# Optimization experiments

Hardware: AMD Instinct MI355X
Metric: run time of the kernel (lower is better)

Reference implementation:

```python
import jax, jax.numpy as jnp
import numpy as np

B, T, E = 2, 2048, 1024
H = 16
DH = E // H  # 64
DFF = 4 * E
EPS = 1e-5


def _layernorm(x, gamma, beta):
    mu = jnp.mean(x, axis=-1, keepdims=True)
    var = jnp.mean((x - mu) ** 2, axis=-1, keepdims=True)
    return (x - mu) * jax.lax.rsqrt(var + EPS) * gamma + beta


def setup_inputs() -> dict:
    key = jax.random.key(0)
    ks = jax.random.split(key, 16)
    s_e = 1.0 / np.sqrt(E)
    s_f = 1.0 / np.sqrt(DFF)
    return {
        "x": jax.random.normal(ks[0], (B, T, E), jnp.float32),
        # per-head QKV projections, stacked over heads [H, E, DH]
        "Wq": jax.random.normal(ks[1], (H, E, DH), jnp.float32) * s_e,
        "bq": jnp.zeros((H, DH), jnp.float32),
        "Wk": jax.random.normal(ks[2], (H, E, DH), jnp.float32) * s_e,
        "bk": jnp.zeros((H, DH), jnp.float32),
        "Wv": jax.random.normal(ks[3], (H, E, DH), jnp.float32) * s_e,
        "bv": jnp.zeros((H, DH), jnp.float32),
        # output projection
        "Wo": jax.random.normal(ks[4], (E, E), jnp.float32) * s_e,
        "bo": jnp.zeros((E,), jnp.float32),
        # feed-forward
        "W1": jax.random.normal(ks[5], (E, DFF), jnp.float32) * s_e,
        "b1": jnp.zeros((DFF,), jnp.float32),
        "W2": jax.random.normal(ks[6], (DFF, E), jnp.float32) * s_f,
        "b2": jnp.zeros((E,), jnp.float32),
        # layernorms
        "gamma1": jnp.ones((E,), jnp.float32),
        "beta1": jnp.zeros((E,), jnp.float32),
        "gamma2": jnp.ones((E,), jnp.float32),
        "beta2": jnp.zeros((E,), jnp.float32),
    }


def reference(x, Wq, bq, Wk, bk, Wv, bv, Wo, bo, W1, b1, W2, b2,
              gamma1, beta1, gamma2, beta2):
    Bc, Tc, Ec = x.shape
    # --- multi-head causal self-attention (dropout = eval/identity) ---
    xn = _layernorm(x, gamma1, beta1)
    q = jnp.einsum('bte,hed->bhtd', xn, Wq) + bq[:, None, :]
    k = jnp.einsum('bte,hed->bhtd', xn, Wk) + bk[:, None, :]
    v = jnp.einsum('bte,hed->bhtd', xn, Wv) + bv[:, None, :]
    scale = 1.0 / np.sqrt(q.shape[-1])
    scores = jnp.einsum('bhtd,bhsd->bhts', q, k) * scale  # [B,H,T,T]
    causal = jnp.tril(jnp.ones((Tc, Tc), bool))
    scores = jnp.where(causal, scores, jnp.float32(-1e9))
    attn = jax.nn.softmax(scores, axis=-1)
    out = jnp.einsum('bhts,bhsd->bhtd', attn, v)          # [B,H,T,DH]
    out = out.transpose(0, 2, 1, 3).reshape(Bc, Tc, Ec)    # concat heads
    out = out @ Wo + bo
    x = x + out
    # --- feed-forward ---
    xn2 = _layernorm(x, gamma2, beta2)
    h = jax.nn.relu(xn2 @ W1 + b1)
    x = x + (h @ W2 + b2)
    return x
```

## Files before the change

kernel.cpp:

```cpp
#include <hip/hip_runtime.h>
#include <stdint.h>

#define BT    4096
#define EDIM  1024
#define TLEN  2048
#define NH    16
#define DHH   64
#define DFFN  4096

typedef short short8 __attribute__((ext_vector_type(8)));
typedef float f32x4  __attribute__((ext_vector_type(4)));

typedef const __attribute__((address_space(1))) unsigned int* gas_ptr;
typedef __attribute__((address_space(3))) unsigned int*       las_ptr;

__device__ __forceinline__ float bf2f(unsigned short u) {
    union { unsigned int i; float f; } c; c.i = ((unsigned int)u) << 16; return c.f;
}
__device__ __forceinline__ unsigned short f2bf(float f) {
    union { float f; unsigned int i; } c; c.f = f;
    unsigned int u = c.i;
    unsigned int r = u + 0x7fffu + ((u >> 16) & 1u);
    return (unsigned short)(r >> 16);
}
__device__ __forceinline__ unsigned short f2bf_trunc(float f) {
    union { float f; unsigned int i; } c; c.f = f;
    return (unsigned short)(c.i >> 16);
}
__device__ __forceinline__ float fexp2(float x) {
#if __has_builtin(__builtin_amdgcn_exp2f)
    return __builtin_amdgcn_exp2f(x);
#else
    return __expf(x * 0.69314718056f);
#endif
}
__device__ __forceinline__ void gload16(const unsigned short* g, unsigned short* l) {
    __builtin_amdgcn_global_load_lds((gas_ptr)g, (las_ptr)l, 16, 0, 0);
}

template<int QKV>
__global__ __launch_bounds__(256) void transpose_kernel(
    const float* src, unsigned short* dst, int Kdim, int srcStride)
{
    __shared__ float T[64][65];
    int t = threadIdx.x;
    int n0 = blockIdx.x * 64, k0 = blockIdx.y * 64;
    int r = t >> 4, c4 = (t & 15) * 4;
    #pragma unroll
    for (int i = 0; i < 4; i++) {
        int rr = r + i * 16;
        const float* p;
        if (QKV) p = src + ((size_t)(n0 >> 6)) * 65536 + (size_t)(k0 + rr) * 64 + c4;
        else     p = src + (size_t)(k0 + rr) * srcStride + n0 + c4;
        float4 v = *(const float4*)p;
        T[c4 + 0][rr] = v.x;
        T[c4 + 1][rr] = v.y;
        T[c4 + 2][rr] = v.z;
        T[c4 + 3][rr] = v.w;
    }
    __syncthreads();
    int rn = t >> 2, ck = (t & 3) * 16;
    short8 o0, o1;
    #pragma unroll
    for (int j = 0; j < 8; j++) o0[j] = (short)f2bf(T[rn][ck + j]);
    #pragma unroll
    for (int j = 0; j < 8; j++) o1[j] = (short)f2bf(T[rn][ck + 8 + j]);
    unsigned short* dp = dst + (size_t)(n0 + rn) * Kdim + k0 + ck;
    *(short8*)dp       = o0;
    *(short8*)(dp + 8) = o1;
}

__global__ __launch_bounds__(256) void transpose_qkv3_kernel(
    const float* __restrict__ Wq, const float* __restrict__ Wk,
    const float* __restrict__ Wv, unsigned short* __restrict__ dstbase)
{
    __shared__ float T[64][65];
    int z = blockIdx.z;
    const float* src = (z == 0) ? Wq : (z == 1) ? Wk : Wv;
    unsigned short* dst = dstbase + (size_t)z * 1048576;
    int t = threadIdx.x;
    int n0 = blockIdx.x * 64, k0 = blockIdx.y * 64;
    int r = t >> 4, c4 = (t & 15) * 4;
    #pragma unroll
    for (int i = 0; i < 4; i++) {
        int rr = r + i * 16;
        const float* p = src + ((size_t)(n0 >> 6)) * 65536 + (size_t)(k0 + rr) * 64 + c4;
        float4 v = *(const float4*)p;
        T[c4 + 0][rr] = v.x;
        T[c4 + 1][rr] = v.y;
        T[c4 + 2][rr] = v.z;
        T[c4 + 3][rr] = v.w;
    }
    __syncthreads();
    int rn = t >> 2, ck = (t & 3) * 16;
    short8 o0, o1;
    #pragma unroll
    for (int j = 0; j < 8; j++) o0[j] = (short)f2bf(T[rn][ck + j]);
    #pragma unroll
    for (int j = 0; j < 8; j++) o1[j] = (short)f2bf(T[rn][ck + 8 + j]);
    unsigned short* dp = dst + (size_t)(n0 + rn) * EDIM + k0 + ck;
    *(short8*)dp       = o0;
    *(short8*)(dp + 8) = o1;
}

__global__ __launch_bounds__(256) void transpose_ffn_kernel(
    const float* __restrict__ W1h, const float* __restrict__ W2h,
    unsigned short* __restrict__ w1t, unsigned short* __restrict__ w2t)
{
    __shared__ float T[64][65];
    int z = blockIdx.z;
    const float* src;
    unsigned short* dst;
    int Kdim, sstride, n0, k0;
    if (z == 0) { src = W1h; dst = w1t; Kdim = 1024; sstride = 4096;
                  n0 = blockIdx.x * 64; k0 = blockIdx.y * 64; }
    else        { src = W2h; dst = w2t; Kdim = 2048; sstride = 1024;
                  n0 = blockIdx.y * 64; k0 = blockIdx.x * 64; }
    int t = threadIdx.x;
    int r = t >> 4, c4 = (t & 15) * 4;
    #pragma unroll
    for (int i = 0; i < 4; i++) {
        int rr = r + i * 16;
        const float* p = src + (size_t)(k0 + rr) * sstride + n0 + c4;
        float4 v = *(const float4*)p;
        T[c4 + 0][rr] = v.x;
        T[c4 + 1][rr] = v.y;
        T[c4 + 2][rr] = v.z;
        T[c4 + 3][rr] = v.w;
    }
    __syncthreads();
    int rn = t >> 2, ck = (t & 3) * 16;
    short8 o0, o1;
    #pragma unroll
    for (int j = 0; j < 8; j++) o0[j] = (short)f2bf(T[rn][ck + j]);
    #pragma unroll
    for (int j = 0; j < 8; j++) o1[j] = (short)f2bf(T[rn][ck + 8 + j]);
    unsigned short* dp = dst + (size_t)(n0 + rn) * Kdim + k0 + ck;
    *(short8*)dp       = o0;
    *(short8*)(dp + 8) = o1;
}

__global__ __launch_bounds__(256) void vtrans_kernel(
    const unsigned short* __restrict__ v, unsigned short* __restrict__ vt)
{
    __shared__ __align__(16) unsigned short T[64][72];
    int bh = blockIdx.x, st = blockIdx.y;
    int t = threadIdx.x;
    int r = t >> 2, c = (t & 3) * 16;
    const unsigned short* src = v + ((size_t)bh * TLEN + st * 64) * DHH;
    short8 a0 = *(const short8*)(src + r * DHH + c);
    short8 a1 = *(const short8*)(src + r * DHH + c + 8);
    *(short8*)&T[r][c]     = a0;
    *(short8*)&T[r][c + 8] = a1;
    __syncthreads();
    int d = t >> 2;
    short8 o0, o1;
    #pragma unroll
    for (int j = 0; j < 8; j++) o0[j] = (short)T[c + j][d];
    #pragma unroll
    for (int j = 0; j < 8; j++) o1[j] = (short)T[c + 8 + j][d];
    unsigned short* dst = vt + ((size_t)bh * DHH + d) * TLEN + st * 64 + c;
    *(short8*)dst       = o0;
    *(short8*)(dst + 8) = o1;
}

__global__ __launch_bounds__(256) void bias_fuse_kernel(
    const float* __restrict__ bq, const float* __restrict__ bk,
    const float* __restrict__ bv, float* __restrict__ dst)
{
    int t = blockIdx.x * 256 + threadIdx.x;
    const float* src = (t < 1024) ? bq : (t < 2048) ? bk : bv;
    dst[t] = src[t & 1023];
}

template<int F32IN>
__global__ __launch_bounds__(256) void ln_fused_kernel(
    const void* __restrict__ x, const float* __restrict__ g,
    const float* __restrict__ b, unsigned short* __restrict__ out)
{
    int row = blockIdx.x, tid = threadIdx.x;
    size_t off = (size_t)row * EDIM + tid * 4;
    float v0, v1, v2, v3;
    if (F32IN) {
        float4 a = *(const float4*)((const float*)x + off);
        v0 = a.x; v1 = a.y; v2 = a.z; v3 = a.w;
    } else {
        ushort4 raw = *(const ushort4*)((const unsigned short*)x + off);
        v0 = bf2f(raw.x); v1 = bf2f(raw.y); v2 = bf2f(raw.z); v3 = bf2f(raw.w);
    }
    float s  = v0 + v1 + v2 + v3;
    float ss = v0*v0 + v1*v1 + v2*v2 + v3*v3;
    #pragma unroll
    for (int o = 1; o < 64; o <<= 1) {
        s  += __shfl_xor(s,  o, 64);
        ss += __shfl_xor(ss, o, 64);
    }
    __shared__ float red[8];
    int wave = tid >> 6;
    if ((tid & 63) == 0) { red[wave*2] = s; red[wave*2+1] = ss; }
    __syncthreads();
    s  = red[0] + red[2] + red[4] + red[6];
    ss = red[1] + red[3] + red[5] + red[7];
    float m  = s * (1.0f / EDIM);
    float rs = rsqrtf(ss * (1.0f / EDIM) - m * m + 1e-5f);
    float4 gv = *(const float4*)(g + tid * 4);
    float4 bv = *(const float4*)(b + tid * 4);
    ushort4 o;
    o.x = f2bf((v0 - m) * rs * gv.x + bv.x);
    o.y = f2bf((v1 - m) * rs * gv.y + bv.y);
    o.z = f2bf((v2 - m) * rs * gv.z + bv.z);
    o.w = f2bf((v3 - m) * rs * gv.w + bv.w);
    *(ushort4*)(out + off) = o;
}

#define V_QKV  0
#define V_WO   1
#define V_FF1  2
#define V_FF2A 3
#define V_FF2B 4

template<int VARIANT, int BN>
__global__ __launch_bounds__(256) void gemm_bt_kernel(
    const unsigned short* A,
    const unsigned short* Bt,
    const float* bias,
    const void* resid,
    void* out,
    int N, int K)
{
    constexpr int NJ = BN / 32;
    __shared__ __align__(16) unsigned short As[128 * 64];
    __shared__ __align__(16) unsigned short Bs[BN * 64];
    int tid  = threadIdx.x;
    int lane = tid & 63, wave = tid >> 6;
    int quad = lane >> 4, l16 = lane & 15;
    int wr = wave >> 1, wc = wave & 1;
    int m0 = blockIdx.y * 128, n0 = blockIdx.x * BN;

    f32x4 acc[4][NJ];
    #pragma unroll
    for (int i = 0; i < 4; i++)
        #pragma unroll
        for (int j = 0; j < NJ; j++) acc[i][j] = (f32x4){0.f, 0.f, 0.f, 0.f};

    int lr = lane >> 3;
    int lc = (lane & 7) * 8;

    for (int k0 = 0; k0 < K; k0 += 64) {
        #pragma unroll
        for (int i = 0; i < 4; i++) {
            int r = (i * 4 + wave) * 8 + lr;
            gload16(A + (size_t)(m0 + r) * K + k0 + lc, &As[(i * 4 + wave) * 512]);
        }
        #pragma unroll
        for (int i = 0; i < NJ; i++) {
            int r = (i * 4 + wave) * 8 + lr;
            gload16(Bt + (size_t)(n0 + r) * K + k0 + lc, &Bs[(i * 4 + wave) * 512]);
        }
        __syncthreads();

        #pragma unroll
        for (int ks = 0; ks < 2; ks++) {
            short8 af[4], bf[NJ];
            #pragma unroll
            for (int i = 0; i < 4; i++)
                af[i] = *(const short8*)(&As[(wr * 64 + i * 16 + l16) * 64 + ks * 32 + quad * 8]);
            #pragma unroll
            for (int j = 0; j < NJ; j++)
                bf[j] = *(const short8*)(&Bs[(wc * (BN / 2) + j * 16 + l16) * 64 + ks * 32 + quad * 8]);
            #pragma unroll
            for (int i = 0; i < 4; i++)
                #pragma unroll
                for (int j = 0; j < NJ; j++)
                    acc[i][j] = __builtin_amdgcn_mfma_f32_16x16x32_bf16(af[i], bf[j], acc[i][j], 0, 0, 0);
        }

        __syncthreads();
    }

    #pragma unroll
    for (int j = 0; j < NJ; j++) {
        int c = n0 + wc * (BN / 2) + j * 16 + l16;
        float bi = (VARIANT == V_FF2A) ? 0.0f : bias[c];
        #pragma unroll
        for (int i = 0; i < 4; i++) {
            #pragma unroll
            for (int r = 0; r < 4; r++) {
                int m = m0 + wr * 64 + i * 16 + quad * 4 + r;
                float val = acc[i][j][r] + bi;
                if (VARIANT == V_WO)
                    val += ((const float*)resid)[(size_t)m * N + c];
                if (VARIANT == V_FF2B)
                    val += bf2f(((const unsigned short*)resid)[(size_t)m * N + c])
                         + ((const float*)out)[(size_t)m * N + c];
                if (VARIANT == V_FF1)
                    val = fmaxf(val, 0.0f);
                if (VARIANT == V_QKV) {
                    int b = m >> 11, t = m & 2047;
                    int mat = c >> 10, cc = c & 1023;
                    int h = cc >> 6, d = cc & 63;
                    ((unsigned short*)out)[(size_t)mat * 4194304 +
                        (((size_t)(b * NH + h)) * TLEN + t) * DHH + d] = f2bf(val);
                } else if (VARIANT == V_FF2A || VARIANT == V_FF2B) {
                    ((float*)out)[(size_t)m * N + c] = val;
                } else {
                    ((unsigned short*)out)[(size_t)m * N + c] = f2bf(val);
                }
            }
        }
    }
}

__global__ __launch_bounds__(256) void attn_kernel(
    const unsigned short* __restrict__ q,
    const unsigned short* __restrict__ k,
    const unsigned short* __restrict__ vt,
    unsigned short* __restrict__ att)
{
    __shared__ __align__(16) unsigned short Ks[128 * 72];
    __shared__ __align__(16) unsigned short Vs[64 * 136];
    __shared__ __align__(16) unsigned short Ps[4][16 * 136];
    int tid  = threadIdx.x;
    int lane = tid & 63, wave = tid >> 6;
    int quad = lane >> 4, l16 = lane & 15;

    int flat = blockIdx.x;
    int xcd  = flat & 7, idx = flat >> 3;
    int bh   = xcd * 4 + (idx >> 5);
    int qt   = 31 - (idx & 31);
    int q0   = qt * 64;
    int qw   = q0 + wave * 16;

    const unsigned short* Qb = q  + ((size_t)bh * TLEN + qw) * DHH;
    const unsigned short* Kb = k  + (size_t)bh * TLEN * DHH;
    const unsigned short* Vb = vt + (size_t)bh * DHH * TLEN;

    short8 aq0 = *(const short8*)(Qb + l16 * DHH + quad * 8);
    short8 aq1 = *(const short8*)(Qb + l16 * DHH + 32 + quad * 8);

    f32x4 o[4];
    #pragma unroll
    for (int n = 0; n < 4; n++) o[n] = (f32x4){0.f, 0.f, 0.f, 0.f};
    f32x4 mrow = {-1e30f, -1e30f, -1e30f, -1e30f};
    f32x4 lrow = {0.f, 0.f, 0.f, 0.f};
    unsigned short* Pw = Ps[wave];
    const float cs = 0.18033688011f;

    int rowK = tid >> 1, colK = (tid & 1) * 32;
    int rowV = tid >> 2, colV = (tid & 3) * 32;

    int nch = (q0 >> 7) + 1;

    short8 ka0, ka1, ka2, ka3, va0, va1, va2, va3;
    {
        const unsigned short* kp = Kb + (size_t)rowK * DHH + colK;
        ka0 = *(const short8*)kp;
        ka1 = *(const short8*)(kp + 8);
        ka2 = *(const short8*)(kp + 16);
        ka3 = *(const short8*)(kp + 24);
        const unsigned short* vp = Vb + (size_t)rowV * TLEN + colV;
        va0 = *(const short8*)vp;
        va1 = *(const short8*)(vp + 8);
        va2 = *(const short8*)(vp + 16);
        va3 = *(const short8*)(vp + 24);
    }

    for (int ch = 0; ch < nch; ch++) {
        int s0 = ch * 128;
        __syncthreads();
        *(short8*)(&Ks[rowK * 72 + colK])       = ka0;
        *(short8*)(&Ks[rowK * 72 + colK + 8])   = ka1;
        *(short8*)(&Ks[rowK * 72 + colK + 16])  = ka2;
        *(short8*)(&Ks[rowK * 72 + colK + 24])  = ka3;
        *(short8*)(&Vs[rowV * 136 + colV])      = va0;
        *(short8*)(&Vs[rowV * 136 + colV + 8])  = va1;
        *(short8*)(&Vs[rowV * 136 + colV + 16]) = va2;
        *(short8*)(&Vs[rowV * 136 + colV + 24]) = va3;
        __syncthreads();

        if (ch + 1 < nch) {
            int s1 = s0 + 128;
            const unsigned short* kp = Kb + (size_t)(s1 + rowK) * DHH + colK;
            ka0 = *(const short8*)kp;
            ka1 = *(const short8*)(kp + 8);
            ka2 = *(const short8*)(kp + 16);
            ka3 = *(const short8*)(kp + 24);
            const unsigned short* vp = Vb + (size_t)rowV * TLEN + s1 + colV;
            va0 = *(const short8*)vp;
            va1 = *(const short8*)(vp + 8);
            va2 = *(const short8*)(vp + 16);
            va3 = *(const short8*)(vp + 24);
        }

        f32x4 S[8];
        #pragma unroll
        for (int n = 0; n < 8; n++) {
            short8 b0 = *(const short8*)(&Ks[(n * 16 + l16) * 72 + quad * 8]);
            short8 b1 = *(const short8*)(&Ks[(n * 16 + l16) * 72 + 32 + quad * 8]);
            f32x4 s = (f32x4){0.f, 0.f, 0.f, 0.f};
            s = __builtin_amdgcn_mfma_f32_16x16x32_bf16(aq0, b0, s, 0, 0, 0);
            s = __builtin_amdgcn_mfma_f32_16x16x32_bf16(aq1, b1, s, 0, 0, 0);
            S[n] = s;
        }
        bool needmask = (s0 + 127 > qw);
        #pragma unroll
        for (int r = 0; r < 4; r++) {
            float xv[8];
            #pragma unroll
            for (int n = 0; n < 8; n++) {
                float xx = S[n][r] * cs;
                if (needmask && (s0 + n * 16 + l16 > qw + quad * 4 + r)) xx = -1e30f;
                xv[n] = xx;
            }
            float mxl = fmaxf(fmaxf(fmaxf(xv[0], xv[1]), fmaxf(xv[2], xv[3])),
                              fmaxf(fmaxf(xv[4], xv[5]), fmaxf(xv[6], xv[7])));
            float used;
            if (__all(mxl <= mrow[r] + 8.0f)) {
                used = mrow[r];
            } else {
                float mx = mxl;
                mx = fmaxf(mx, __shfl_xor(mx, 1, 64));
                mx = fmaxf(mx, __shfl_xor(mx, 2, 64));
                mx = fmaxf(mx, __shfl_xor(mx, 4, 64));
                mx = fmaxf(mx, __shfl_xor(mx, 8, 64));
                float mnew  = fmaxf(mrow[r], mx);
                float alpha = fexp2(mrow[r] - mnew);
                lrow[r] *= alpha;
                o[0][r] *= alpha; o[1][r] *= alpha;
                o[2][r] *= alpha; o[3][r] *= alpha;
                mrow[r] = mnew;
                used = mnew;
            }
            float ps = 0.f;
            int prow = (quad * 4 + r) * 136;
            #pragma unroll
            for (int n = 0; n < 8; n++) {
                float p = fexp2(xv[n] - used);
                ps += p;
                Pw[prow + n * 16 + l16] = f2bf_trunc(p);
            }
            lrow[r] += ps;
        }
        short8 ap[4];
        #pragma unroll
        for (int ks = 0; ks < 4; ks++)
            ap[ks] = *(const short8*)(Pw + l16 * 136 + ks * 32 + quad * 8);
        #pragma unroll
        for (int n = 0; n < 4; n++) {
            #pragma unroll
            for (int ks = 0; ks < 4; ks++) {
                short8 b = *(const short8*)(&Vs[(n * 16 + l16) * 136 + ks * 32 + quad * 8]);
                o[n] = __builtin_amdgcn_mfma_f32_16x16x32_bf16(ap[ks], b, o[n], 0, 0, 0);
            }
        }
    }

    int bidx = bh >> 4, hh = bh & 15;
    #pragma unroll
    for (int r = 0; r < 4; r++) {
        float ls = lrow[r];
        ls += __shfl_xor(ls, 1, 64);
        ls += __shfl_xor(ls, 2, 64);
        ls += __shfl_xor(ls, 4, 64);
        ls += __shfl_xor(ls, 8, 64);
        float inv = 1.0f / ls;
        int t = qw + quad * 4 + r;
        size_t rowoff = ((size_t)(bidx * TLEN + t)) * EDIM + hh * 64;
        #pragma unroll
        for (int n = 0; n < 4; n++)
            att[rowoff + n * 16 + l16] = f2bf(o[n][r] * inv);
    }
}

extern "C" void kernel_launch(void* const* d_in, const int* in_sizes, int n_in,
                              void* d_out, int out_size, void* d_ws, size_t ws_size,
                              hipStream_t stream)
{
    (void)in_sizes; (void)n_in; (void)out_size; (void)ws_size;
    const float* x   = (const float*)d_in[0];
    const float* Wq  = (const float*)d_in[1];
    const float* bq  = (const float*)d_in[2];
    const float* Wk  = (const float*)d_in[3];
    const float* bk  = (const float*)d_in[4];
    const float* Wv  = (const float*)d_in[5];
    const float* bv  = (const float*)d_in[6];
    const float* Wo  = (const float*)d_in[7];
    const float* bo  = (const float*)d_in[8];
    const float* W1  = (const float*)d_in[9];
    const float* b1  = (const float*)d_in[10];
    const float* W2  = (const float*)d_in[11];
    const float* b2  = (const float*)d_in[12];
    const float* g1  = (const float*)d_in[13];
    const float* be1 = (const float*)d_in[14];
    const float* g2  = (const float*)d_in[15];
    const float* be2 = (const float*)d_in[16];

    unsigned short* ws  = (unsigned short*)d_ws;
    unsigned short* xn  = ws;
    unsigned short* vtg = ws;
    unsigned short* qb  = ws + 4194304;
    unsigned short* kb  = ws + 8388608;
    unsigned short* vb  = ws + 12582912;
    unsigned short* wqt = ws + 16777216;
    unsigned short* att = ws + 16777216;
    unsigned short* x1  = ws + 4194304;
    unsigned short* wot = ws + 8388608;
    unsigned short* w1t = ws + 8388608;
    unsigned short* w2t = ws + 10485760;
    unsigned short* hb  = ws + 12582912;
    float* biasf = (float*)(ws + 19922944);

    dim3 gT64(16, 16);
    dim3 gE(EDIM / 64, BT / 128);
    dim3 gQKV(3072 / 128, BT / 128);
    dim3 gF(2048 / 128, BT / 128);

    transpose_qkv3_kernel<<<dim3(16, 16, 3), 256, 0, stream>>>(Wq, Wk, Wv, wqt);
    bias_fuse_kernel<<<dim3(12), 256, 0, stream>>>(bq, bk, bv, biasf);

    ln_fused_kernel<1><<<BT, 256, 0, stream>>>(x, g1, be1, xn);

    gemm_bt_kernel<V_QKV, 128><<<gQKV, 256, 0, stream>>>(xn, wqt, biasf, nullptr, qb, 3072, EDIM);

    vtrans_kernel<<<dim3(NH * 2, TLEN / 64), 256, 0, stream>>>(vb, vtg);

    attn_kernel<<<dim3(1024), 256, 0, stream>>>(qb, kb, vtg, att);

    transpose_kernel<0><<<gT64, 256, 0, stream>>>(Wo, wot, EDIM, EDIM);
    gemm_bt_kernel<V_WO, 64><<<gE, 256, 0, stream>>>(att, wot, bo, x, x1, EDIM, EDIM);

    ln_fused_kernel<0><<<BT, 256, 0, stream>>>(x1, g2, be2, xn);

    transpose_ffn_kernel<<<dim3(32, 16, 2), 256, 0, stream>>>(W1, W2, w1t, w2t);
    gemm_bt_kernel<V_FF1, 128><<<gF, 256, 0, stream>>>(xn, w1t, b1, nullptr, hb, 2048, EDIM);
    gemm_bt_kernel<V_FF2A, 64><<<gE, 256, 0, stream>>>(hb, w2t, nullptr, nullptr, d_out, EDIM, 2048);
    transpose_ffn_kernel<<<dim3(32, 16, 2), 256, 0, stream>>>(W1 + 2048, W2 + (size_t)2048 * EDIM, w1t, w2t);
    gemm_bt_kernel<V_FF1, 128><<<gF, 256, 0, stream>>>(xn, w1t, b1 + 2048, nullptr, hb, 2048, EDIM);
    gemm_bt_kernel<V_FF2B, 64><<<gE, 256, 0, stream>>>(hb, w2t, b2, x1, d_out, EDIM, 2048);
}
```

Measured before the change: 433.5 us.

## Double attention query tile to 128 rows with 8 waves sharing K/V chunks

The attention kernel now runs 512 threads (8 waves) per block, each block covering 128 query rows instead of 64, so every K/V chunk loaded into shared memory serves twice as many queries. This halves the global K/V traffic and staging work per query. The softmax and PV step is split into two 64-key halves, and a wave skips the half lying entirely above the causal diagonal, which removes wasted exp and MFMA work on fully masked keys. In exchange there are half as many blocks (512), larger blocks and more waves per barrier, which can lower occupancy and worsen load balance across the causal triangle.

```diff
diff --git a/kernel.cpp b/kernel.cpp
--- a/kernel.cpp
+++ b/kernel.cpp
@@ -311,7 +311,7 @@
     }
 }
 
-__global__ __launch_bounds__(256) void attn_kernel(
+__global__ __launch_bounds__(512) void attn_kernel(
     const unsigned short* __restrict__ q,
     const unsigned short* __restrict__ k,
     const unsigned short* __restrict__ vt,
@@ -319,16 +319,16 @@
 {
     __shared__ __align__(16) unsigned short Ks[128 * 72];
     __shared__ __align__(16) unsigned short Vs[64 * 136];
-    __shared__ __align__(16) unsigned short Ps[4][16 * 136];
+    __shared__ __align__(16) unsigned short Ps[8][16 * 72];
     int tid  = threadIdx.x;
     int lane = tid & 63, wave = tid >> 6;
     int quad = lane >> 4, l16 = lane & 15;
 
     int flat = blockIdx.x;
     int xcd  = flat & 7, idx = flat >> 3;
-    int bh   = xcd * 4 + (idx >> 5);
-    int qt   = 31 - (idx & 31);
-    int q0   = qt * 64;
+    int bh   = xcd * 4 + (idx >> 4);
+    int qt   = 15 - (idx & 15);
+    int q0   = qt * 128;
     int qw   = q0 + wave * 16;
 
     const unsigned short* Qb = q  + ((size_t)bh * TLEN + qw) * DHH;
@@ -346,36 +346,28 @@
     unsigned short* Pw = Ps[wave];
     const float cs = 0.18033688011f;
 
-    int rowK = tid >> 1, colK = (tid & 1) * 32;
-    int rowV = tid >> 2, colV = (tid & 3) * 32;
-
-    int nch = (q0 >> 7) + 1;
-
-    short8 ka0, ka1, ka2, ka3, va0, va1, va2, va3;
+    int rowK = tid >> 2, colK = (tid & 3) * 16;
+    int rowV = tid >> 3, colV = (tid & 7) * 16;
+
+    int nch = qt + 1;
+
+    short8 ka0, ka1, va0, va1;
     {
         const unsigned short* kp = Kb + (size_t)rowK * DHH + colK;
         ka0 = *(const short8*)kp;
         ka1 = *(const short8*)(kp + 8);
-        ka2 = *(const short8*)(kp + 16);
-        ka3 = *(const short8*)(kp + 24);
         const unsigned short* vp = Vb + (size_t)rowV * TLEN + colV;
         va0 = *(const short8*)vp;
         va1 = *(const short8*)(vp + 8);
-        va2 = *(const short8*)(vp + 16);
-        va3 = *(const short8*)(vp + 24);
     }
 
     for (int ch = 0; ch < nch; ch++) {
         int s0 = ch * 128;
         __syncthreads();
-        *(short8*)(&Ks[rowK * 72 + colK])       = ka0;
-        *(short8*)(&Ks[rowK * 72 + colK + 8])   = ka1;
-        *(short8*)(&Ks[rowK * 72 + colK + 16])  = ka2;
-        *(short8*)(&Ks[rowK * 72 + colK + 24])  = ka3;
-        *(short8*)(&Vs[rowV * 136 + colV])      = va0;
-        *(short8*)(&Vs[rowV * 136 + colV + 8])  = va1;
-        *(short8*)(&Vs[rowV * 136 + colV + 16]) = va2;
-        *(short8*)(&Vs[rowV * 136 + colV + 24]) = va3;
+        *(short8*)(&Ks[rowK * 72 + colK])      = ka0;
+        *(short8*)(&Ks[rowK * 72 + colK + 8])  = ka1;
+        *(short8*)(&Vs[rowV * 136 + colV])     = va0;
+        *(short8*)(&Vs[rowV * 136 + colV + 8]) = va1;
         __syncthreads();
 
         if (ch + 1 < nch) {
@@ -383,13 +375,9 @@
             const unsigned short* kp = Kb + (size_t)(s1 + rowK) * DHH + colK;
             ka0 = *(const short8*)kp;
             ka1 = *(const short8*)(kp + 8);
-            ka2 = *(const short8*)(kp + 16);
-            ka3 = *(const short8*)(kp + 24);
             const unsigned short* vp = Vb + (size_t)rowV * TLEN + s1 + colV;
             va0 = *(const short8*)vp;
             va1 = *(const short8*)(vp + 8);
-            va2 = *(const short8*)(vp + 16);
-            va3 = *(const short8*)(vp + 24);
         }
 
         f32x4 S[8];
@@ -402,55 +390,58 @@
             s = __builtin_amdgcn_mfma_f32_16x16x32_bf16(aq1, b1, s, 0, 0, 0);
             S[n] = s;
         }
-        bool needmask = (s0 + 127 > qw);
-        #pragma unroll
-        for (int r = 0; r < 4; r++) {
-            float xv[8];
+
+        #pragma unroll
+        for (int h = 0; h < 2; h++) {
+            int sh = s0 + h * 64;
+            if (sh > qw + 15) continue;
+            bool needmask = (sh + 63 > qw);
             #pragma unroll
-            for (int n = 0; n < 8; n++) {
-                float xx = S[n][r] * cs;
-                if (needmask && (s0 + n * 16 + l16 > qw + quad * 4 + r)) xx = -1e30f;
-                xv[n] = xx;
+            for (int r = 0; r < 4; r++) {
+                float xv[4];
+                #pragma unroll
+                for (int n = 0; n < 4; n++) {
+                    float xx = S[h * 4 + n][r] * cs;
+                    if (needmask && (sh + n * 16 + l16 > qw + quad * 4 + r)) xx = -1e30f;
+                    xv[n] = xx;
+                }
+                float mxl = fmaxf(fmaxf(xv[0], xv[1]), fmaxf(xv[2], xv[3]));
+                float used;
+                if (__all(mxl <= mrow[r] + 8.0f)) {
+                    used = mrow[r];
+                } else {
+                    float mx = mxl;
+                    mx = fmaxf(mx, __shfl_xor(mx, 1, 64));
+                    mx = fmaxf(mx, __shfl_xor(mx, 2, 64));
+                    mx = fmaxf(mx, __shfl_xor(mx, 4, 64));
+                    mx = fmaxf(mx, __shfl_xor(mx, 8, 64));
+                    float mnew  = fmaxf(mrow[r], mx);
+                    float alpha = fexp2(mrow[r] - mnew);
+                    lrow[r] *= alpha;
+                    o[0][r] *= alpha; o[1][r] *= alpha;
+                    o[2][r] *= alpha; o[3][r] *= alpha;
+                    mrow[r] = mnew;
+                    used = mnew;
+                }
+                float ps = 0.f;
+                int prow = (quad * 4 + r) * 72;
+                #pragma unroll
+                for (int n = 0; n < 4; n++) {
+                    float p = fexp2(xv[n] - used);
+                    ps += p;
+                    Pw[prow + n * 16 + l16] = f2bf_trunc(p);
+                }
+                lrow[r] += ps;
             }
-            float mxl = fmaxf(fmaxf(fmaxf(xv[0], xv[1]), fmaxf(xv[2], xv[3])),
-                              fmaxf(fmaxf(xv[4], xv[5]), fmaxf(xv[6], xv[7])));
-            float used;
-            if (__all(mxl <= mrow[r] + 8.0f)) {
-                used = mrow[r];
-            } else {
-                float mx = mxl;
-                mx = fmaxf(mx, __shfl_xor(mx, 1, 64));
-                mx = fmaxf(mx, __shfl_xor(mx, 2, 64));
-                mx = fmaxf(mx, __shfl_xor(mx, 4, 64));
-                mx = fmaxf(mx, __shfl_xor(mx, 8, 64));
-                float mnew  = fmaxf(mrow[r], mx);
-                float alpha = fexp2(mrow[r] - mnew);
-                lrow[r] *= alpha;
-                o[0][r] *= alpha; o[1][r] *= alpha;
-                o[2][r] *= alpha; o[3][r] *= alpha;
-                mrow[r] = mnew;
-                used = mnew;
-            }
-            float ps = 0.f;
-            int prow = (quad * 4 + r) * 136;
+            short8 ap0 = *(const short8*)(Pw + l16 * 72 + quad * 8);
+            short8 ap1 = *(const short8*)(Pw + l16 * 72 + 32 + quad * 8);
             #pragma unroll
-            for (int n = 0; n < 8; n++) {
-                float p = fexp2(xv[n] - used);
-                ps += p;
-                Pw[prow + n * 16 + l16] = f2bf_trunc(p);
-            }
-            lrow[r] += ps;
-        }
-        short8 ap[4];
-        #pragma unroll
-        for (int ks = 0; ks < 4; ks++)
-            ap[ks] = *(const short8*)(Pw + l16 * 136 + ks * 32 + quad * 8);
-        #pragma unroll
-        for (int n = 0; n < 4; n++) {
-            #pragma unroll
-            for (int ks = 0; ks < 4; ks++) {
-                short8 b = *(const short8*)(&Vs[(n * 16 + l16) * 136 + ks * 32 + quad * 8]);
-                o[n] = __builtin_amdgcn_mfma_f32_16x16x32_bf16(ap[ks], b, o[n], 0, 0, 0);
+            for (int n = 0; n < 4; n++) {
+                const unsigned short* vrow = &Vs[(n * 16 + l16) * 136 + h * 64];
+                short8 b0 = *(const short8*)(vrow + quad * 8);
+                short8 b1 = *(const short8*)(vrow + 32 + quad * 8);
+                o[n] = __builtin_amdgcn_mfma_f32_16x16x32_bf16(ap0, b0, o[n], 0, 0, 0);
+                o[n] = __builtin_amdgcn_mfma_f32_16x16x32_bf16(ap1, b1, o[n], 0, 0, 0);
             }
         }
     }
@@ -524,7 +515,7 @@
 
     vtrans_kernel<<<dim3(NH * 2, TLEN / 64), 256, 0, stream>>>(vb, vtg);
 
-    attn_kernel<<<dim3(1024), 256, 0, stream>>>(qb, kb, vtg, att);
+    attn_kernel<<<dim3(512), 512, 0, stream>>>(qb, kb, vtg, att);
 
     transpose_kernel<0><<<gT64, 256, 0, stream>>>(Wo, wot, EDIM, EDIM);
     gemm_bt_kernel<V_WO, 64><<<gE, 256, 0, stream>>>(att, wot, bo, x, x1, EDIM, EDIM);
```

Measured after the change: 443.6 us. +2.3%, slower.
